# Performance work log

Hardware: AMD Instinct MI355X
Metric: run time of the kernel (lower is better)

Reference implementation:

```python
import jax, jax.numpy as jnp
import numpy as np

NUM_EMBEDDINGS = 512
EMBEDDING_DIM = 64
COMMITMENT_COST = 0.25


def setup_inputs() -> dict:
    key = jax.random.key(0)
    k_in, k_cb = jax.random.split(key)
    inputs = jax.random.normal(k_in, (32, EMBEDDING_DIM, 64, 64), dtype=jnp.float32)
    # nn.Embedding weight initialized uniform(-1/K, 1/K)
    codebook = jax.random.uniform(
        k_cb, (NUM_EMBEDDINGS, EMBEDDING_DIM), dtype=jnp.float32,
        minval=-1.0 / NUM_EMBEDDINGS, maxval=1.0 / NUM_EMBEDDINGS)
    return {"inputs": inputs, "codebook": codebook}


def reference(inputs, codebook):
    N, D, H, W = inputs.shape
    # [N, H, W, D] -> [N*H*W, D]
    flat = jnp.transpose(inputs, (0, 2, 3, 1)).reshape(-1, D)
    # Squared euclidean distances (argmin identical to cdist's euclidean argmin)
    d2 = (jnp.sum(flat * flat, axis=1, keepdims=True)
          - 2.0 * flat @ codebook.T
          + jnp.sum(codebook * codebook, axis=1))  # [N*H*W, K]
    encoding_index = jnp.argmin(d2, axis=1)  # [N*H*W]
    quantized = codebook[encoding_index]      # gather [N*H*W, D]
    quantized = quantized.reshape(N, H, W, D).transpose(0, 3, 1, 2)  # [N, D, H, W]
    e_latent_loss = jnp.mean((jax.lax.stop_gradient(quantized) - inputs) ** 2)
    q_latent_loss = jnp.mean((quantized - jax.lax.stop_gradient(inputs)) ** 2)
    c_loss = q_latent_loss + COMMITMENT_COST * e_latent_loss
    # straight-through estimator
    quantized_st = inputs + jax.lax.stop_gradient(quantized - inputs)
    return (c_loss, quantized_st)
```

## Files before the change

### kernel.cpp

```cpp
#include <hip/hip_runtime.h>

#define DIM 64
#define HW 4096
#define NELEM 8388608.0f
#define NBLK 2048

typedef __attribute__((ext_vector_type(8))) short short8;
typedef __attribute__((ext_vector_type(4))) float f32x4;

__device__ __forceinline__ unsigned short f2bf(float f) {
  unsigned int u = __builtin_bit_cast(unsigned int, f);
  u += 0x7fffu + ((u >> 16) & 1u);
  return (unsigned short)(u >> 16);
}

__device__ __forceinline__ float wave_sum(float v) {
  #pragma unroll
  for (int off = 32; off >= 1; off >>= 1) v += __shfl_xor(v, off);
  return v;
}


__global__ void vq_prep(const float* __restrict__ CB,
                        unsigned short* __restrict__ aFg,
                        float* __restrict__ cn) {
  const int t = threadIdx.x;
  const int s = blockIdx.x * 512 + t;
  const int chunk = s >> 7, ks = (s >> 6) & 1, ls = s & 63;
  const int code = chunk * 16 + (ls & 15);
  const int d0 = ks * 32 + (ls >> 4) * 8;
  const float* cp = CB + code * DIM + d0;
  float4 u0 = *(const float4*)cp;
  float4 u1 = *(const float4*)(cp + 4);
  short8 p;
  p[0]=(short)f2bf(-2.f*u0.x); p[1]=(short)f2bf(-2.f*u0.y);
  p[2]=(short)f2bf(-2.f*u0.z); p[3]=(short)f2bf(-2.f*u0.w);
  p[4]=(short)f2bf(-2.f*u1.x); p[5]=(short)f2bf(-2.f*u1.y);
  p[6]=(short)f2bf(-2.f*u1.z); p[7]=(short)f2bf(-2.f*u1.w);
  *(short8*)&aFg[s * 8] = p;
  if (blockIdx.x == 0) {
    const float* c2 = CB + t * DIM;
    float sn = 0.f;
    #pragma unroll
    for (int i = 0; i < 16; ++i) {
      float4 u = *(const float4*)(c2 + i * 4);
      sn += u.x*u.x + u.y*u.y + u.z*u.z + u.w*u.w;
    }
    cn[t] = sn;
  }
}

__global__ __launch_bounds__(256, 4)
void vq_main(const float* __restrict__ X, const float* __restrict__ CB,
             const unsigned short* __restrict__ aFg,
             const float* __restrict__ cng,
             float* __restrict__ out,
             float* __restrict__ pA, float* __restrict__ pB) {
  __shared__ unsigned short Xt[64][66];
  __shared__ float mW[4][64];
  __shared__ float red[8];

  const int t   = threadIdx.x;
  const int bid = blockIdx.x;
  const int L   = ((bid & 7) << 8) | (bid >> 3);
  const int n   = L >> 6;
  const int hw0 = (L & 63) << 6;
  const int wv  = t >> 6, lane = t & 63;
  const int g   = lane >> 4, lcol = lane & 15;

  const float* Xg = X + n * (DIM * HW) + hw0;

  float sx2 = 0.f;
  #pragma unroll
  for (int i = 0; i < 4; ++i) {
    int q   = i * 256 + t;
    int row = q >> 4;
    int c4  = (q & 15) << 2;
    const float4 v = *(const float4*)(Xg + row * HW + c4);
    sx2 += v.x*v.x + v.y*v.y + v.z*v.z + v.w*v.w;
    ushort4 h;
    h.x = f2bf(v.x); h.y = f2bf(v.y); h.z = f2bf(v.z); h.w = f2bf(v.w);
    *(ushort4*)&Xt[row][c4] = h;
  }
  __syncthreads();

  short8 bfrag[4][2];
  #pragma unroll
  for (int cb = 0; cb < 4; ++cb) {
    int col = cb * 16 + lcol;
    #pragma unroll
    for (int ks = 0; ks < 2; ++ks) {
      short8 v;
      #pragma unroll
      for (int j = 0; j < 8; ++j) v[j] = (short)Xt[ks*32 + g*8 + j][col];
      bfrag[cb][ks] = v;
    }
  }

  float m1[4];
  #pragma unroll
  for (int cb = 0; cb < 4; ++cb) m1[cb] = 3.0e38f;

  const int chunk0 = wv * 8;
  #pragma unroll 4
  for (int i = 0; i < 8; ++i) {
    const int chunk = chunk0 + i;
    const short8 a0 = *(const short8*)&aFg[((chunk*2 + 0) * 64 + lane) * 8];
    const short8 a1 = *(const short8*)&aFg[((chunk*2 + 1) * 64 + lane) * 8];
    const int codebase = chunk * 16 + g * 4;
    const f32x4 cn = *(const f32x4*)&cng[codebase];
    #pragma unroll
    for (int cb = 0; cb < 4; ++cb) {
      f32x4 acc = cn;
      acc = __builtin_amdgcn_mfma_f32_16x16x32_bf16(a0, bfrag[cb][0], acc, 0, 0, 0);
      acc = __builtin_amdgcn_mfma_f32_16x16x32_bf16(a1, bfrag[cb][1], acc, 0, 0, 0);
      #pragma unroll
      for (int r = 0; r < 4; ++r) {
        unsigned int vb = __builtin_bit_cast(unsigned int, acc[r]);
        vb = (vb & 0xFFFFFE00u) | (unsigned)(codebase + r);
        m1[cb] = fminf(m1[cb], __builtin_bit_cast(float, vb));
      }
    }
  }

  #pragma unroll
  for (int cb = 0; cb < 4; ++cb) {
    m1[cb] = fminf(m1[cb], __shfl_xor(m1[cb], 16));
    m1[cb] = fminf(m1[cb], __shfl_xor(m1[cb], 32));
    if (g == 0) mW[wv][cb * 16 + lcol] = m1[cb];
  }
  __syncthreads();

  const float p = fminf(fminf(mW[0][lane], mW[1][lane]),
                        fminf(mW[2][lane], mW[3][lane]));
  const unsigned int b = __builtin_bit_cast(unsigned int, p);
  const int k = (int)(b & 511u);
  const float minval = __builtin_bit_cast(float, b & 0xFFFFFE00u);

  const float* cq = CB + k * DIM + wv * 16;
  float* op = out + 1 + n * (DIM * HW) + hw0 + lane;
  #pragma unroll
  for (int i = 0; i < 4; ++i) {
    float4 u = *(const float4*)(cq + i * 4);
    op[(wv*16 + i*4 + 0) * HW] = u.x;
    op[(wv*16 + i*4 + 1) * HW] = u.y;
    op[(wv*16 + i*4 + 2) * HW] = u.z;
    op[(wv*16 + i*4 + 3) * HW] = u.w;
  }

  float w1 = wave_sum(sx2);
  if (lane == 0) red[wv] = w1;
  if (wv == 0) {
    float w2 = wave_sum(minval);
    if (lane == 0) red[4] = w2;
  }
  __syncthreads();
  if (t == 0) {
    pA[bid] = red[0] + red[1] + red[2] + red[3];
    pB[bid] = red[4];
  }
}

__global__ void vq_fin(const float* __restrict__ pA,
                       const float* __restrict__ pB,
                       float* __restrict__ out) {
  const int t = threadIdx.x;
  float4 a = *(const float4*)&pA[t * 4];
  float4 c = *(const float4*)&pB[t * 4];
  float v = a.x + a.y + a.z + a.w + c.x + c.y + c.z + c.w;
  v = wave_sum(v);
  __shared__ float r[8];
  if ((t & 63) == 0) r[t >> 6] = v;
  __syncthreads();
  if (t == 0) {
    float s = 0.f;
    #pragma unroll
    for (int i = 0; i < 8; ++i) s += r[i];
    out[0] = 1.25f * s * (1.0f / NELEM);
  }
}

extern "C" void kernel_launch(void* const* d_in, const int* in_sizes, int n_in,
                              void* d_out, int out_size, void* d_ws, size_t ws_size,
                              hipStream_t stream) {
  const float* X  = (const float*)d_in[0];
  const float* CB = (const float*)d_in[1];
  float* out = (float*)d_out;
  char* ws = (char*)d_ws;
  unsigned short* aFg = (unsigned short*)ws;
  float* cn = (float*)(ws + 65536);
  float* pA = (float*)(ws + 67584);
  float* pB = (float*)(ws + 75776);
  (void)in_sizes; (void)n_in; (void)out_size; (void)ws_size;

  vq_prep<<<8, 512, 0, stream>>>(CB, aFg, cn);
  vq_main<<<NBLK, 256, 0, stream>>>(X, CB, aFg, cn, out, pA, pB);
  vq_fin<<<1, 512, 0, stream>>>(pA, pB, out);
}
```

Before: 35.59 us.

## Process two 128-pixel tiles per block with software-pipelined loads

Each block now handles two 128-pixel tiles instead of one 64-pixel tile, with a quarter as many blocks. The second tile's global loads are issued before the first tile's MFMA distance and argmin pass, so memory latency overlaps compute. The packed bf16 fragments are written to LDS in a swizzled layout that allows vector short8 reads. Loads and stores also become nontemporal. The cost is higher register pressure (occupancy hint lowered to 2) and fewer blocks to spread across CUs.

```diff
diff --git a/kernel.cpp b/kernel.cpp
--- a/kernel.cpp
+++ b/kernel.cpp
@@ -3,10 +3,11 @@
 #define DIM 64
 #define HW 4096
 #define NELEM 8388608.0f
-#define NBLK 2048
+#define NBLK 512
 
 typedef __attribute__((ext_vector_type(8))) short short8;
 typedef __attribute__((ext_vector_type(4))) float f32x4;
+typedef __attribute__((ext_vector_type(2))) float f32x2;
 
 __device__ __forceinline__ unsigned short f2bf(float f) {
   unsigned int u = __builtin_bit_cast(unsigned int, f);
@@ -50,124 +51,168 @@
   }
 }
 
-__global__ __launch_bounds__(256, 4)
+__global__ __launch_bounds__(256, 2)
 void vq_main(const float* __restrict__ X, const float* __restrict__ CB,
              const unsigned short* __restrict__ aFg,
              const float* __restrict__ cng,
              float* __restrict__ out,
              float* __restrict__ pA, float* __restrict__ pB) {
-  __shared__ unsigned short Xt[64][66];
-  __shared__ float mW[4][64];
+  __shared__ __align__(16) unsigned short XF[16 * 64 * 8];
+  __shared__ float mW[4][128];
   __shared__ float red[8];
 
   const int t   = threadIdx.x;
   const int bid = blockIdx.x;
-  const int L   = ((bid & 7) << 8) | (bid >> 3);
-  const int n   = L >> 6;
-  const int hw0 = (L & 63) << 6;
+  const int Lp  = ((bid & 7) << 6) | (bid >> 3);
+  const int tile0 = Lp * 2;
+  const int n   = tile0 >> 5;
+  const int hwA = (tile0 & 31) << 7;
+  const int hwB = hwA + 128;
   const int wv  = t >> 6, lane = t & 63;
   const int g   = lane >> 4, lcol = lane & 15;
-
-  const float* Xg = X + n * (DIM * HW) + hw0;
-
-  float sx2 = 0.f;
-  #pragma unroll
-  for (int i = 0; i < 4; ++i) {
-    int q   = i * 256 + t;
-    int row = q >> 4;
-    int c4  = (q & 15) << 2;
-    const float4 v = *(const float4*)(Xg + row * HW + c4);
-    sx2 += v.x*v.x + v.y*v.y + v.z*v.z + v.w*v.w;
-    ushort4 h;
-    h.x = f2bf(v.x); h.y = f2bf(v.y); h.z = f2bf(v.z); h.w = f2bf(v.w);
-    *(ushort4*)&Xt[row][c4] = h;
-  }
-  __syncthreads();
-
-  short8 bfrag[4][2];
-  #pragma unroll
-  for (int cb = 0; cb < 4; ++cb) {
-    int col = cb * 16 + lcol;
-    #pragma unroll
-    for (int ks = 0; ks < 2; ++ks) {
-      short8 v;
-      #pragma unroll
-      for (int j = 0; j < 8; ++j) v[j] = (short)Xt[ks*32 + g*8 + j][col];
-      bfrag[cb][ks] = v;
-    }
-  }
-
-  float m1[4];
-  #pragma unroll
-  for (int cb = 0; cb < 4; ++cb) m1[cb] = 3.0e38f;
-
-  const int chunk0 = wv * 8;
-  #pragma unroll 4
-  for (int i = 0; i < 8; ++i) {
-    const int chunk = chunk0 + i;
-    const short8 a0 = *(const short8*)&aFg[((chunk*2 + 0) * 64 + lane) * 8];
-    const short8 a1 = *(const short8*)&aFg[((chunk*2 + 1) * 64 + lane) * 8];
-    const int codebase = chunk * 16 + g * 4;
-    const f32x4 cn = *(const f32x4*)&cng[codebase];
-    #pragma unroll
-    for (int cb = 0; cb < 4; ++cb) {
-      f32x4 acc = cn;
-      acc = __builtin_amdgcn_mfma_f32_16x16x32_bf16(a0, bfrag[cb][0], acc, 0, 0, 0);
-      acc = __builtin_amdgcn_mfma_f32_16x16x32_bf16(a1, bfrag[cb][1], acc, 0, 0, 0);
-      #pragma unroll
-      for (int r = 0; r < 4; ++r) {
-        unsigned int vb = __builtin_bit_cast(unsigned int, acc[r]);
-        vb = (vb & 0xFFFFFE00u) | (unsigned)(codebase + r);
-        m1[cb] = fminf(m1[cb], __builtin_bit_cast(float, vb));
-      }
-    }
-  }
-
-  #pragma unroll
-  for (int cb = 0; cb < 4; ++cb) {
-    m1[cb] = fminf(m1[cb], __shfl_xor(m1[cb], 16));
-    m1[cb] = fminf(m1[cb], __shfl_xor(m1[cb], 32));
-    if (g == 0) mW[wv][cb * 16 + lcol] = m1[cb];
-  }
-  __syncthreads();
-
-  const float p = fminf(fminf(mW[0][lane], mW[1][lane]),
-                        fminf(mW[2][lane], mW[3][lane]));
-  const unsigned int b = __builtin_bit_cast(unsigned int, p);
-  const int k = (int)(b & 511u);
-  const float minval = __builtin_bit_cast(float, b & 0xFFFFFE00u);
-
-  const float* cq = CB + k * DIM + wv * 16;
-  float* op = out + 1 + n * (DIM * HW) + hw0 + lane;
-  #pragma unroll
-  for (int i = 0; i < 4; ++i) {
-    float4 u = *(const float4*)(cq + i * 4);
-    op[(wv*16 + i*4 + 0) * HW] = u.x;
-    op[(wv*16 + i*4 + 1) * HW] = u.y;
-    op[(wv*16 + i*4 + 2) * HW] = u.z;
-    op[(wv*16 + i*4 + 3) * HW] = u.w;
-  }
+  const int db8 = t >> 5;
+  const int cq  = t & 31;
+  const int kss = db8 >> 2, gs = db8 & 3;
+  const float* Xbase = X + n * (DIM * HW);
+
+  float sx2 = 0.f, msum = 0.f;
+  f32x4 v[8];
+
+#define LOADX(hw0)                                                          \
+  _Pragma("unroll")                                                         \
+  for (int j = 0; j < 8; ++j)                                               \
+    v[j] = __builtin_nontemporal_load(                                      \
+        (const f32x4*)(Xbase + (hw0) + (db8 * 8 + j) * HW + cq * 4));
+
+#define PACKX()                                                             \
+  _Pragma("unroll")                                                         \
+  for (int j = 0; j < 8; ++j)                                               \
+    sx2 += v[j].x*v[j].x + v[j].y*v[j].y + v[j].z*v[j].z + v[j].w*v[j].w;   \
+  _Pragma("unroll")                                                         \
+  for (int ci = 0; ci < 4; ++ci) {                                          \
+    const int c    = cq * 4 + ci;                               \
+    const int slot = ((c >> 4) * 2 + kss) * 64 + gs * 16 + (c & 15);        \
+    const int swz  = slot ^ ((slot >> 3) & 7);                              \
+    short8 w;                                                               \
+    _Pragma("unroll")                                                       \
+    for (int j = 0; j < 8; ++j)                                             \
+      w[j] = (short)f2bf(v[j][ci]);                                         \
+    *(short8*)&XF[swz * 8] = w;                                             \
+  }
+
+#define COMPUTE_MINRED()                                                    \
+  {                                                                         \
+    const int swzl = lane ^ ((lane >> 3) & 7);                              \
+    short8 bfrag[2][4][2];                                                  \
+    _Pragma("unroll")                                                       \
+    for (int h = 0; h < 2; ++h)                                             \
+      _Pragma("unroll")                                                     \
+      for (int cb2 = 0; cb2 < 4; ++cb2)                                     \
+        _Pragma("unroll")                                                   \
+        for (int ks = 0; ks < 2; ++ks)                                      \
+          bfrag[h][cb2][ks] =                                               \
+              *(const short8*)&XF[(((h*4+cb2)*2 + ks)*64 + swzl) * 8];      \
+    float m1[8];                                                            \
+    _Pragma("unroll")                                                       \
+    for (int cb = 0; cb < 8; ++cb) m1[cb] = 3.0e38f;                        \
+    const int chunk0 = wv * 8;                                              \
+    _Pragma("unroll 2")                                                     \
+    for (int i = 0; i < 8; ++i) {                                           \
+      const int chunk = chunk0 + i;                                         \
+      const short8 a0 = *(const short8*)&aFg[((chunk*2+0)*64 + lane) * 8];  \
+      const short8 a1 = *(const short8*)&aFg[((chunk*2+1)*64 + lane) * 8];  \
+      const int codebase = chunk * 16 + g * 4;                              \
+      const f32x4 cn = *(const f32x4*)&cng[codebase];                       \
+      _Pragma("unroll")                                                     \
+      for (int h = 0; h < 2; ++h) {                                         \
+        _Pragma("unroll")                                                   \
+        for (int cb2 = 0; cb2 < 4; ++cb2) {                                 \
+          f32x4 acc = cn;                                                   \
+          acc = __builtin_amdgcn_mfma_f32_16x16x32_bf16(a0, bfrag[h][cb2][0], acc, 0, 0, 0); \
+          acc = __builtin_amdgcn_mfma_f32_16x16x32_bf16(a1, bfrag[h][cb2][1], acc, 0, 0, 0); \
+          _Pragma("unroll")                                                 \
+          for (int r = 0; r < 4; ++r) {                                     \
+            unsigned int vb = __builtin_bit_cast(unsigned int, acc[r]);     \
+            vb = (vb & 0xFFFFFE00u) | ((unsigned)(codebase + r) & 0x1FFu);  \
+            m1[h*4+cb2] = fminf(m1[h*4+cb2], __builtin_bit_cast(float, vb));\
+          }                                                                 \
+        }                                                                   \
+      }                                                                     \
+    }                                                                       \
+    _Pragma("unroll")                                                       \
+    for (int cb = 0; cb < 8; ++cb) {                                        \
+      m1[cb] = fminf(m1[cb], __shfl_xor(m1[cb], 16));                       \
+      m1[cb] = fminf(m1[cb], __shfl_xor(m1[cb], 32));                       \
+      if (g == 0) mW[wv][cb * 16 + lcol] = m1[cb];                          \
+    }                                                                       \
+  }
+
+#define EPILOGUE(hw0)                                                       \
+  _Pragma("unroll")                                                         \
+  for (int h = 0; h < 2; ++h) {                                             \
+    const int c = h * 64 + lane;                                            \
+    const float p = fminf(fminf(mW[0][c], mW[1][c]),                        \
+                          fminf(mW[2][c], mW[3][c]));                       \
+    const unsigned int b = __builtin_bit_cast(unsigned int, p);             \
+    const int k = (int)(b & 511u);                                          \
+    msum += __builtin_bit_cast(float, b & 0xFFFFFE00u);                     \
+    const float* cqp = CB + k * DIM + wv * 16;           \
+    float* op = out + 1 + n * (DIM * HW) + (hw0) + c;                       \
+    _Pragma("unroll")                                                       \
+    for (int i = 0; i < 4; ++i) {                                           \
+      float4 u = *(const float4*)(cqp + i * 4);                             \
+      __builtin_nontemporal_store(u.x, &op[(wv*16 + i*4 + 0) * HW]);        \
+      __builtin_nontemporal_store(u.y, &op[(wv*16 + i*4 + 1) * HW]);        \
+      __builtin_nontemporal_store(u.z, &op[(wv*16 + i*4 + 2) * HW]);        \
+      __builtin_nontemporal_store(u.w, &op[(wv*16 + i*4 + 3) * HW]);        \
+    }                                                                       \
+  }
+
+  LOADX(hwA);
+  PACKX();
+  __syncthreads();
+
+  LOADX(hwB);
+  __builtin_amdgcn_sched_barrier(0);
+
+  COMPUTE_MINRED();
+  __syncthreads();
+
+  PACKX();
+  EPILOGUE(hwA);
+  asm volatile("s_waitcnt lgkmcnt(0)" ::: "memory");
+  __builtin_amdgcn_sched_barrier(0);
+  __builtin_amdgcn_s_barrier();
+  __builtin_amdgcn_sched_barrier(0);
+
+  COMPUTE_MINRED();
+  __syncthreads();
+
+  EPILOGUE(hwB);
 
   float w1 = wave_sum(sx2);
   if (lane == 0) red[wv] = w1;
   if (wv == 0) {
-    float w2 = wave_sum(minval);
+    float w2 = wave_sum(msum);
     if (lane == 0) red[4] = w2;
   }
-  __syncthreads();
+  asm volatile("s_waitcnt lgkmcnt(0)" ::: "memory");
+  __builtin_amdgcn_s_barrier();
   if (t == 0) {
     pA[bid] = red[0] + red[1] + red[2] + red[3];
     pB[bid] = red[4];
   }
+#undef LOADX
+#undef PACKX
+#undef COMPUTE_MINRED
+#undef EPILOGUE
 }
 
 __global__ void vq_fin(const float* __restrict__ pA,
                        const float* __restrict__ pB,
                        float* __restrict__ out) {
   const int t = threadIdx.x;
-  float4 a = *(const float4*)&pA[t * 4];
-  float4 c = *(const float4*)&pB[t * 4];
-  float v = a.x + a.y + a.z + a.w + c.x + c.y + c.z + c.w;
+  float v = pA[t] + pB[t];
   v = wave_sum(v);
   __shared__ float r[8];
   if ((t & 63) == 0) r[t >> 6] = v;
```

Measured after the change: 34.91 us. About the same (-1.9%).
